# Kernel optimization log

Hardware: AMD Instinct MI355X
Metric: run time of the kernel (lower is better)

The kernel has to match this reference:

```python
import jax, jax.numpy as jnp
import numpy as np

B, M, N = 8, 8192, 8192  # batch, input neurons, output neurons
SPIKE_CAP = 0.9          # VPRTempo caps spike amplitude at 0.9


def setup_inputs() -> dict:
    key = jax.random.key(0)
    k0, k1, k2, k3 = jax.random.split(key, 4)
    # pre-synaptic spike amplitudes in [0, 1)
    pre_spikes = jax.random.uniform(k0, (B, 1, M), dtype=jnp.float32)
    # combined excitatory+inhibitory weights
    W = jax.random.normal(k1, (M, N), dtype=jnp.float32) * 0.01
    # per-neuron thresholds, uniform in thr_range = [0, 0.5]
    thr = jax.random.uniform(k2, (B, 1, N), dtype=jnp.float32) * 0.5
    # per-neuron constant input, uniform in const_inp = [0, 0.1]
    const_inp = jax.random.uniform(k3, (B, 1, N), dtype=jnp.float32) * 0.1
    return {"pre_spikes": pre_spikes, "W": W, "thr": thr, "const_inp": const_inp}


def reference(pre_spikes, W, thr, const_inp):
    # membrane potential: weighted pre-synaptic spikes + constant input
    x = jnp.einsum('bom,mn->bon', pre_spikes, W) + const_inp  # [B,1,N]
    # spike generation: amplitude above threshold, clamped to [0, 0.9]
    spikes = jnp.clip(x - thr, 0.0, SPIKE_CAP)
    return spikes
```

## Files before the change

kernel.cpp:

```cpp
#include <hip/hip_runtime.h>


constexpr int Mdim = 8192;
constexpr int Ndim = 8192;
constexpr int Bdim = 8;
constexpr int KSLICES = 32;
constexpr int KROWS = Mdim / KSLICES;

__global__ __launch_bounds__(256, 1) void snn_fused(
    const float* __restrict__ pre,
    const float* __restrict__ W,
    const float* __restrict__ thr,
    const float* __restrict__ cst,
    float* __restrict__ out)
{
    __shared__ float partial[KSLICES * Bdim * 32];

    const int tid = threadIdx.x;
    const int tx  = tid & 7;
    const int ty  = tid >> 3;
    const int colBase = blockIdx.x * 32;
    const int col = colBase + tx * 4;
    const int m0  = ty * KROWS;

    float acc[Bdim][4];
#pragma unroll
    for (int b = 0; b < Bdim; ++b)
#pragma unroll
        for (int c = 0; c < 4; ++c) acc[b][c] = 0.0f;

#pragma unroll 2
    for (int m = m0; m < m0 + KROWS; m += 4) {
        float4 p[Bdim];
#pragma unroll
        for (int b = 0; b < Bdim; ++b)
            p[b] = *reinterpret_cast<const float4*>(pre + b * Mdim + m);

        float4 w0 = *reinterpret_cast<const float4*>(W + (size_t)(m + 0) * Ndim + col);
        float4 w1 = *reinterpret_cast<const float4*>(W + (size_t)(m + 1) * Ndim + col);
        float4 w2 = *reinterpret_cast<const float4*>(W + (size_t)(m + 2) * Ndim + col);
        float4 w3 = *reinterpret_cast<const float4*>(W + (size_t)(m + 3) * Ndim + col);

#pragma unroll
        for (int b = 0; b < Bdim; ++b) {
            acc[b][0] = fmaf(p[b].x, w0.x, acc[b][0]);
            acc[b][1] = fmaf(p[b].x, w0.y, acc[b][1]);
            acc[b][2] = fmaf(p[b].x, w0.z, acc[b][2]);
            acc[b][3] = fmaf(p[b].x, w0.w, acc[b][3]);

            acc[b][0] = fmaf(p[b].y, w1.x, acc[b][0]);
            acc[b][1] = fmaf(p[b].y, w1.y, acc[b][1]);
            acc[b][2] = fmaf(p[b].y, w1.z, acc[b][2]);
            acc[b][3] = fmaf(p[b].y, w1.w, acc[b][3]);

            acc[b][0] = fmaf(p[b].z, w2.x, acc[b][0]);
            acc[b][1] = fmaf(p[b].z, w2.y, acc[b][1]);
            acc[b][2] = fmaf(p[b].z, w2.z, acc[b][2]);
            acc[b][3] = fmaf(p[b].z, w2.w, acc[b][3]);

            acc[b][0] = fmaf(p[b].w, w3.x, acc[b][0]);
            acc[b][1] = fmaf(p[b].w, w3.y, acc[b][1]);
            acc[b][2] = fmaf(p[b].w, w3.z, acc[b][2]);
            acc[b][3] = fmaf(p[b].w, w3.w, acc[b][3]);
        }
    }

#pragma unroll
    for (int b = 0; b < Bdim; ++b) {
        float4* dst = reinterpret_cast<float4*>(&partial[(ty * Bdim + b) * 32 + tx * 4]);
        *dst = make_float4(acc[b][0], acc[b][1], acc[b][2], acc[b][3]);
    }
    __syncthreads();

    const int ob = tid >> 5;
    const int oc = tid & 31;
    float s = 0.0f;
#pragma unroll
    for (int t = 0; t < KSLICES; ++t)
        s += partial[(t * Bdim + ob) * 32 + oc];

    const int oi = ob * Ndim + colBase + oc;
    float x = s + cst[oi] - thr[oi];
    x = fminf(fmaxf(x, 0.0f), 0.9f);
    out[oi] = x;
}

extern "C" void kernel_launch(void* const* d_in, const int* in_sizes, int n_in,
                              void* d_out, int out_size, void* d_ws, size_t ws_size,
                              hipStream_t stream) {
    const float* pre = (const float*)d_in[0];
    const float* W   = (const float*)d_in[1];
    const float* thr = (const float*)d_in[2];
    const float* cst = (const float*)d_in[3];
    float* out = (float*)d_out;

    dim3 grid(Ndim / 32);
    dim3 block(256);
    hipLaunchKernelGGL(snn_fused, grid, block, 0, stream, pre, W, thr, cst, out);
}
```

Before: 408.5 us.

## Split GEMV into two-stage split-K with global partials and reduction kernel

Replaces the single fused kernel, which used 256 blocks each reducing 32 in-block K-slices through shared memory, with a two-kernel split-K scheme. Stage one runs a 8x64 grid where each block reads a contiguous 1024-column-wide strip of W across 128 rows, giving fully coalesced 4KB row reads, and writes per-chunk partial sums to the workspace. Stage two sums the 64 partials and applies the constant, threshold and clamp. This is meant to improve W streaming and occupancy across the GPU, at the cost of 16MB of extra partial-sum traffic and a second launch.

```diff
diff --git a/kernel.cpp b/kernel.cpp
--- a/kernel.cpp
+++ b/kernel.cpp
@@ -4,85 +4,80 @@
 constexpr int Mdim = 8192;
 constexpr int Ndim = 8192;
 constexpr int Bdim = 8;
-constexpr int KSLICES = 32;
-constexpr int KROWS = Mdim / KSLICES;
+constexpr int KCH  = 64;
+constexpr int ROWS = Mdim / KCH;
+constexpr int TILE_N = 1024;
+constexpr float CAP = 0.9f;
 
-__global__ __launch_bounds__(256, 1) void snn_fused(
+__global__ __launch_bounds__(256, 2) void snn_stage1(
     const float* __restrict__ pre,
     const float* __restrict__ W,
+    float* __restrict__ part)
+{
+    const int t   = threadIdx.x;
+    const int col = blockIdx.x * TILE_N + t * 4;
+    const int r0  = blockIdx.y * ROWS;
+
+    float4 acc[Bdim];
+#pragma unroll
+    for (int b = 0; b < Bdim; ++b) acc[b] = make_float4(0.f, 0.f, 0.f, 0.f);
+
+    for (int r = r0; r < r0 + ROWS; r += 8) {
+        float4 w[8];
+#pragma unroll
+        for (int j = 0; j < 8; ++j)
+            w[j] = *reinterpret_cast<const float4*>(W + (size_t)(r + j) * Ndim + col);
+
+        float4 pA[Bdim], pB[Bdim];
+#pragma unroll
+        for (int b = 0; b < Bdim; ++b) {
+            pA[b] = *reinterpret_cast<const float4*>(pre + b * Mdim + r);
+            pB[b] = *reinterpret_cast<const float4*>(pre + b * Mdim + r + 4);
+        }
+
+#pragma unroll
+        for (int b = 0; b < Bdim; ++b) {
+            float4 a = acc[b];
+            a.x = fmaf(pA[b].x, w[0].x, a.x); a.y = fmaf(pA[b].x, w[0].y, a.y);
+            a.z = fmaf(pA[b].x, w[0].z, a.z); a.w = fmaf(pA[b].x, w[0].w, a.w);
+            a.x = fmaf(pA[b].y, w[1].x, a.x); a.y = fmaf(pA[b].y, w[1].y, a.y);
+            a.z = fmaf(pA[b].y, w[1].z, a.z); a.w = fmaf(pA[b].y, w[1].w, a.w);
+            a.x = fmaf(pA[b].z, w[2].x, a.x); a.y = fmaf(pA[b].z, w[2].y, a.y);
+            a.z = fmaf(pA[b].z, w[2].z, a.z); a.w = fmaf(pA[b].z, w[2].w, a.w);
+            a.x = fmaf(pA[b].w, w[3].x, a.x); a.y = fmaf(pA[b].w, w[3].y, a.y);
+            a.z = fmaf(pA[b].w, w[3].z, a.z); a.w = fmaf(pA[b].w, w[3].w, a.w);
+            a.x = fmaf(pB[b].x, w[4].x, a.x); a.y = fmaf(pB[b].x, w[4].y, a.y);
+            a.z = fmaf(pB[b].x, w[4].z, a.z); a.w = fmaf(pB[b].x, w[4].w, a.w);
+            a.x = fmaf(pB[b].y, w[5].x, a.x); a.y = fmaf(pB[b].y, w[5].y, a.y);
+            a.z = fmaf(pB[b].y, w[5].z, a.z); a.w = fmaf(pB[b].y, w[5].w, a.w);
+            a.x = fmaf(pB[b].z, w[6].x, a.x); a.y = fmaf(pB[b].z, w[6].y, a.y);
+            a.z = fmaf(pB[b].z, w[6].z, a.z); a.w = fmaf(pB[b].z, w[6].w, a.w);
+            a.x = fmaf(pB[b].w, w[7].x, a.x); a.y = fmaf(pB[b].w, w[7].y, a.y);
+            a.z = fmaf(pB[b].w, w[7].z, a.z); a.w = fmaf(pB[b].w, w[7].w, a.w);
+            acc[b] = a;
+        }
+    }
+
+    float* pslice = part + (size_t)blockIdx.y * (Bdim * Ndim);
+#pragma unroll
+    for (int b = 0; b < Bdim; ++b)
+        *reinterpret_cast<float4*>(pslice + (size_t)b * Ndim + col) = acc[b];
+}
+
+__global__ __launch_bounds__(256, 4) void snn_stage2(
+    const float* __restrict__ part,
     const float* __restrict__ thr,
     const float* __restrict__ cst,
     float* __restrict__ out)
 {
-    __shared__ float partial[KSLICES * Bdim * 32];
-
-    const int tid = threadIdx.x;
-    const int tx  = tid & 7;
-    const int ty  = tid >> 3;
-    const int colBase = blockIdx.x * 32;
-    const int col = colBase + tx * 4;
-    const int m0  = ty * KROWS;
-
-    float acc[Bdim][4];
+    const int i = blockIdx.x * 256 + threadIdx.x;
+    float s = 0.f;
 #pragma unroll
-    for (int b = 0; b < Bdim; ++b)
-#pragma unroll
-        for (int c = 0; c < 4; ++c) acc[b][c] = 0.0f;
-
-#pragma unroll 2
-    for (int m = m0; m < m0 + KROWS; m += 4) {
-        float4 p[Bdim];
-#pragma unroll
-        for (int b = 0; b < Bdim; ++b)
-            p[b] = *reinterpret_cast<const float4*>(pre + b * Mdim + m);
-
-        float4 w0 = *reinterpret_cast<const float4*>(W + (size_t)(m + 0) * Ndim + col);
-        float4 w1 = *reinterpret_cast<const float4*>(W + (size_t)(m + 1) * Ndim + col);
-        float4 w2 = *reinterpret_cast<const float4*>(W + (size_t)(m + 2) * Ndim + col);
-        float4 w3 = *reinterpret_cast<const float4*>(W + (size_t)(m + 3) * Ndim + col);
-
-#pragma unroll
-        for (int b = 0; b < Bdim; ++b) {
-            acc[b][0] = fmaf(p[b].x, w0.x, acc[b][0]);
-            acc[b][1] = fmaf(p[b].x, w0.y, acc[b][1]);
-            acc[b][2] = fmaf(p[b].x, w0.z, acc[b][2]);
-            acc[b][3] = fmaf(p[b].x, w0.w, acc[b][3]);
-
-            acc[b][0] = fmaf(p[b].y, w1.x, acc[b][0]);
-            acc[b][1] = fmaf(p[b].y, w1.y, acc[b][1]);
-            acc[b][2] = fmaf(p[b].y, w1.z, acc[b][2]);
-            acc[b][3] = fmaf(p[b].y, w1.w, acc[b][3]);
-
-            acc[b][0] = fmaf(p[b].z, w2.x, acc[b][0]);
-            acc[b][1] = fmaf(p[b].z, w2.y, acc[b][1]);
-            acc[b][2] = fmaf(p[b].z, w2.z, acc[b][2]);
-            acc[b][3] = fmaf(p[b].z, w2.w, acc[b][3]);
-
-            acc[b][0] = fmaf(p[b].w, w3.x, acc[b][0]);
-            acc[b][1] = fmaf(p[b].w, w3.y, acc[b][1]);
-            acc[b][2] = fmaf(p[b].w, w3.z, acc[b][2]);
-            acc[b][3] = fmaf(p[b].w, w3.w, acc[b][3]);
-        }
-    }
-
-#pragma unroll
-    for (int b = 0; b < Bdim; ++b) {
-        float4* dst = reinterpret_cast<float4*>(&partial[(ty * Bdim + b) * 32 + tx * 4]);
-        *dst = make_float4(acc[b][0], acc[b][1], acc[b][2], acc[b][3]);
-    }
-    __syncthreads();
-
-    const int ob = tid >> 5;
-    const int oc = tid & 31;
-    float s = 0.0f;
-#pragma unroll
-    for (int t = 0; t < KSLICES; ++t)
-        s += partial[(t * Bdim + ob) * 32 + oc];
-
-    const int oi = ob * Ndim + colBase + oc;
-    float x = s + cst[oi] - thr[oi];
-    x = fminf(fmaxf(x, 0.0f), 0.9f);
-    out[oi] = x;
+    for (int k = 0; k < KCH; ++k)
+        s += part[(size_t)k * (Bdim * Ndim) + i];
+    float x = s + cst[i] - thr[i];
+    x = fminf(fmaxf(x, 0.f), CAP);
+    out[i] = x;
 }
 
 extern "C" void kernel_launch(void* const* d_in, const int* in_sizes, int n_in,
@@ -92,9 +87,12 @@
     const float* W   = (const float*)d_in[1];
     const float* thr = (const float*)d_in[2];
     const float* cst = (const float*)d_in[3];
-    float* out = (float*)d_out;
+    float* out  = (float*)d_out;
+    float* part = (float*)d_ws;
 
-    dim3 grid(Ndim / 32);
-    dim3 block(256);
-    hipLaunchKernelGGL(snn_fused, grid, block, 0, stream, pre, W, thr, cst, out);
+    dim3 g1(Ndim / TILE_N, KCH);
+    hipLaunchKernelGGL(snn_stage1, g1, dim3(256), 0, stream, pre, W, part);
+
+    dim3 g2((Bdim * Ndim) / 256);
+    hipLaunchKernelGGL(snn_stage2, g2, dim3(256), 0, stream, part, thr, cst, out);
 }
```

Result: faster. 379.0 us (-7.2%).
